# Kernel optimization log

Hardware: AMD Instinct MI355X
Metric: run time of the kernel (lower is better)

Reference implementation:

```python
import jax, jax.numpy as jnp
import numpy as np

P = 5            # assets (fixed by 5x5 MLP)
K = 4            # stacked layers
LB, UB = 0.0, 0.5
RF = 1.03
B = 524288       # batch size
ALPHA, OMEGA, BETA, MU = 0.1, 0.05, 0.05, 0.01
MAX_REBAL_ITERS = 8  # water-filling clamp loop converges in a few iters for P=5


def setup_inputs() -> dict:
    key = jax.random.key(0)
    k1, k2, k3, k4 = jax.random.split(key, 4)
    x1 = jax.random.uniform(k1, (B,), dtype=jnp.float32)                 # wealth per sample
    x2 = jax.random.uniform(k2, (B, P, P), dtype=jnp.float32)            # prev covariance
    eps = jax.random.normal(k3, (K, B, P), dtype=jnp.float32)            # N(0,I) draw per layer
    W = jax.random.normal(k4, (K, 3, P, P), dtype=jnp.float32) * 0.5     # 3 bias-free Linear(5,5) per layer
    return {"x1": x1, "x2": x2, "eps": eps, "W": W}


def _rebalance(w):
    """Vectorized clamp/redistribute loop over the whole batch. w: (B,P)."""
    old = w
    new = jnp.clip(w, LB, UB)
    done = jnp.zeros(w.shape[0], dtype=bool)

    def body(carry, _):
        old, new, done = carry
        leftover = jnp.sum(old - new, axis=1, keepdims=True)            # (B,1)
        masked = jnp.where(new != UB, new, 0.0)                          # non-capped weights
        new2 = new + leftover * masked / jnp.sum(masked, axis=1, keepdims=True)
        cont = jnp.any(new2 > UB, axis=1)                                # (B,)
        new3 = jnp.where(cont[:, None], jnp.clip(new2, LB, UB), new2)
        # freeze rows that already converged
        old_n = jnp.where(done[:, None], old, new2)
        new_n = jnp.where(done[:, None], new, new3)
        return (old_n, new_n, done | ~cont), None

    (_, new, _), _ = jax.lax.scan(body, (old, new, done), None, length=MAX_REBAL_ITERS)
    return new


def reference(x1, x2, eps, W):
    # Replicates the original bug: every StackLayer consumes the ORIGINAL
    # (x1, x2); only the last layer's output is returned.
    for k in range(K):
        Ce = jnp.einsum('bij,bj->bi', x2, eps[k])                        # prev_cov @ eps, (B,P)
        curr_cov = OMEGA + ALPHA * x2 + BETA * (Ce ** 2)[:, None, :]     # (B,P,P), row-broadcast
        R = MU + Ce                                                      # (B,P)
        h = R
        for l in range(3):                                               # torch Linear: x @ W.T
            h = jnp.tanh(h @ W[k, l].T)
        wts = jax.nn.softmax(h, axis=1)
        wts = _rebalance(wts)
        wealth = jnp.sum(x1[:, None] * wts * (1.0 + R) * RF, axis=1)     # (B,)
    return wealth, curr_cov
```

## Files before the change

### kernel.cpp

```cpp
#include <hip/hip_runtime.h>
#include <cmath>

#define P 5
#define LBV 0.0f
#define UBV 0.5f
#define RFV 1.03f
#define ALPHA 0.1f
#define OMEGA 0.05f
#define BETA 0.05f
#define MU 0.01f
#define NTHR 256

__device__ __forceinline__ float fast_tanh(float x) {
    float ax = fabsf(x);
    float t  = __expf(-2.0f * ax);
    float r  = (1.0f - t) * __builtin_amdgcn_rcpf(1.0f + t);
    return copysignf(r, x);
}

__global__ __launch_bounds__(NTHR) void portfolio_kernel(
    const float* __restrict__ x1,
    const float* __restrict__ x2,
    const float* __restrict__ eps,
    const float* __restrict__ W,
    float* __restrict__ out, int B)
{
    __shared__ float sW[3 * P * P];
    __shared__ float sX2[NTHR * P * P];
    __shared__ float sE[NTHR * P];

    const int tid = threadIdx.x;
    const int b0  = blockIdx.x * NTHR;

    if (tid < 3 * P * P) sW[tid] = W[3 * 3 * P * P + tid];

    const float* gx2 = x2 + (size_t)b0 * (P * P);
    #pragma unroll
    for (int i = 0; i < P * P; ++i)
        sX2[i * NTHR + tid] = gx2[i * NTHR + tid];

    const float* ge = eps + (size_t)3 * B * P + (size_t)b0 * P;
    #pragma unroll
    for (int i = 0; i < P; ++i)
        sE[i * NTHR + tid] = ge[i * NTHR + tid];

    __syncthreads();

    float* row = &sX2[tid * (P * P)];
    float r2[P * P];
    #pragma unroll
    for (int i = 0; i < P * P; ++i) r2[i] = row[i];

    float e[P];
    #pragma unroll
    for (int j = 0; j < P; ++j) e[j] = sE[tid * P + j];

    float Ce[P];
    #pragma unroll
    for (int i = 0; i < P; ++i) {
        float s = 0.0f;
        #pragma unroll
        for (int j = 0; j < P; ++j) s = fmaf(r2[i * P + j], e[j], s);
        Ce[i] = s;
    }

    float R[P], h[P];
    #pragma unroll
    for (int i = 0; i < P; ++i) { R[i] = MU + Ce[i]; h[i] = R[i]; }

    #pragma unroll
    for (int l = 0; l < 3; ++l) {
        float hn[P];
        #pragma unroll
        for (int i = 0; i < P; ++i) {
            float s = 0.0f;
            #pragma unroll
            for (int j = 0; j < P; ++j) s = fmaf(h[j], sW[l * P * P + i * P + j], s);
            hn[i] = fast_tanh(s);
        }
        #pragma unroll
        for (int i = 0; i < P; ++i) h[i] = hn[i];
    }

    float w[P], ssum = 0.0f;
    #pragma unroll
    for (int i = 0; i < P; ++i) { w[i] = __expf(h[i]); ssum += w[i]; }
    float rs = __builtin_amdgcn_rcpf(ssum);
    #pragma unroll
    for (int i = 0; i < P; ++i) w[i] *= rs;

    float oldv[P], nw[P];
    #pragma unroll
    for (int i = 0; i < P; ++i) {
        oldv[i] = w[i];
        nw[i]   = fminf(fmaxf(w[i], LBV), UBV);
    }
    #pragma unroll
    for (int it = 0; it < 8; ++it) {
        float leftover = 0.0f;
        #pragma unroll
        for (int i = 0; i < P; ++i) leftover += oldv[i] - nw[i];
        float mk[P], msum = 0.0f;
        #pragma unroll
        for (int i = 0; i < P; ++i) {
            mk[i] = (nw[i] != UBV) ? nw[i] : 0.0f;
            msum += mk[i];
        }
        float scale = leftover * __builtin_amdgcn_rcpf(msum);
        float n2[P];
        #pragma unroll
        for (int i = 0; i < P; ++i) n2[i] = fmaf(scale, mk[i], nw[i]);
        bool cont = false;
        #pragma unroll
        for (int i = 0; i < P; ++i) cont = cont || (n2[i] > UBV);
        #pragma unroll
        for (int i = 0; i < P; ++i) {
            oldv[i] = n2[i];
            nw[i]   = cont ? fminf(fmaxf(n2[i], LBV), UBV) : n2[i];
        }
        if (!cont) break;
    }

    float x1v = x1[b0 + tid];
    float ws = 0.0f;
    #pragma unroll
    for (int i = 0; i < P; ++i) ws = fmaf(nw[i], 1.0f + R[i], ws);
    out[b0 + tid] = x1v * ws * RFV;

    float ce2[P];
    #pragma unroll
    for (int j = 0; j < P; ++j) ce2[j] = Ce[j] * Ce[j];
    #pragma unroll
    for (int i = 0; i < P; ++i) {
        #pragma unroll
        for (int j = 0; j < P; ++j)
            row[i * P + j] = fmaf(BETA, ce2[j], fmaf(ALPHA, r2[i * P + j], OMEGA));
    }

    __syncthreads();

    float* gout = out + B + (size_t)b0 * (P * P);
    #pragma unroll
    for (int i = 0; i < P * P; ++i)
        gout[i * NTHR + tid] = sX2[i * NTHR + tid];
}

extern "C" void kernel_launch(void* const* d_in, const int* in_sizes, int n_in,
                              void* d_out, int out_size, void* d_ws, size_t ws_size,
                              hipStream_t stream) {
    const float* x1  = (const float*)d_in[0];
    const float* x2  = (const float*)d_in[1];
    const float* eps = (const float*)d_in[2];
    const float* W   = (const float*)d_in[3];
    float* out = (float*)d_out;
    const int B = in_sizes[0];
    const int blocks = B / NTHR;
    portfolio_kernel<<<blocks, NTHR, 0, stream>>>(x1, x2, eps, W, out, B);
}
```

Before: 134.5 us.

## Stage covariance via direct global-to-LDS loads and write output straight to global

Replaces the per-thread global-to-shared copy of the 256x25 covariance tile with global_load_lds 16-byte async copies straight into LDS. Eps and x1 are now loaded directly into registers per thread, and the weight matrices are read from global memory instead of shared memory. The output covariance is written directly from registers with a strided per-thread store, which drops the second barrier and LDS round trip but gives uncoalesced 100-byte-strided stores. It also adds a min-blocks-per-CU launch bound of 5 to raise occupancy.

```diff
diff --git a/kernel.cpp b/kernel.cpp
--- a/kernel.cpp
+++ b/kernel.cpp
@@ -11,6 +11,9 @@
 #define MU 0.01f
 #define NTHR 256
 
+#define AS1 __attribute__((address_space(1)))
+#define AS3 __attribute__((address_space(3)))
+
 __device__ __forceinline__ float fast_tanh(float x) {
     float ax = fabsf(x);
     float t  = __expf(-2.0f * ax);
@@ -18,42 +21,42 @@
     return copysignf(r, x);
 }
 
-__global__ __launch_bounds__(NTHR) void portfolio_kernel(
+__global__ __launch_bounds__(NTHR, 5) void portfolio_kernel(
     const float* __restrict__ x1,
     const float* __restrict__ x2,
     const float* __restrict__ eps,
     const float* __restrict__ W,
     float* __restrict__ out, int B)
 {
-    __shared__ float sW[3 * P * P];
     __shared__ float sX2[NTHR * P * P];
-    __shared__ float sE[NTHR * P];
 
-    const int tid = threadIdx.x;
-    const int b0  = blockIdx.x * NTHR;
+    const int tid  = threadIdx.x;
+    const int b0   = blockIdx.x * NTHR;
+    const int lane = tid & 63;
+    const int wv   = tid >> 6;
 
-    if (tid < 3 * P * P) sW[tid] = W[3 * 3 * P * P + tid];
+    float x1v = x1[b0 + tid];
+    const float* ge = eps + (size_t)3 * B * P + (size_t)(b0 + tid) * P;
+    float e[P];
+    #pragma unroll
+    for (int j = 0; j < P; ++j) e[j] = ge[j];
 
     const float* gx2 = x2 + (size_t)b0 * (P * P);
     #pragma unroll
-    for (int i = 0; i < P * P; ++i)
-        sX2[i * NTHR + tid] = gx2[i * NTHR + tid];
-
-    const float* ge = eps + (size_t)3 * B * P + (size_t)b0 * P;
-    #pragma unroll
-    for (int i = 0; i < P; ++i)
-        sE[i * NTHR + tid] = ge[i * NTHR + tid];
-
+    for (int i = 0; i < 6; ++i) {
+        int c = (i * 4 + wv) * 256;
+        __builtin_amdgcn_global_load_lds((const AS1 void*)(gx2 + c + lane * 4),
+                                         (AS3 void*)(&sX2[c]), 16, 0, 0);
+    }
+    if (wv == 0) {
+        __builtin_amdgcn_global_load_lds((const AS1 void*)(gx2 + 6144 + lane * 4),
+                                         (AS3 void*)(&sX2[6144]), 16, 0, 0);
+    }
     __syncthreads();
 
-    float* row = &sX2[tid * (P * P)];
     float r2[P * P];
     #pragma unroll
-    for (int i = 0; i < P * P; ++i) r2[i] = row[i];
-
-    float e[P];
-    #pragma unroll
-    for (int j = 0; j < P; ++j) e[j] = sE[tid * P + j];
+    for (int i = 0; i < P * P; ++i) r2[i] = sX2[tid * (P * P) + i];
 
     float Ce[P];
     #pragma unroll
@@ -68,6 +71,7 @@
     #pragma unroll
     for (int i = 0; i < P; ++i) { R[i] = MU + Ce[i]; h[i] = R[i]; }
 
+    const float* Wl = W + 3 * 3 * P * P;
     #pragma unroll
     for (int l = 0; l < 3; ++l) {
         float hn[P];
@@ -75,7 +79,7 @@
         for (int i = 0; i < P; ++i) {
             float s = 0.0f;
             #pragma unroll
-            for (int j = 0; j < P; ++j) s = fmaf(h[j], sW[l * P * P + i * P + j], s);
+            for (int j = 0; j < P; ++j) s = fmaf(h[j], Wl[l * P * P + i * P + j], s);
             hn[i] = fast_tanh(s);
         }
         #pragma unroll
@@ -121,7 +125,6 @@
         if (!cont) break;
     }
 
-    float x1v = x1[b0 + tid];
     float ws = 0.0f;
     #pragma unroll
     for (int i = 0; i < P; ++i) ws = fmaf(nw[i], 1.0f + R[i], ws);
@@ -130,19 +133,13 @@
     float ce2[P];
     #pragma unroll
     for (int j = 0; j < P; ++j) ce2[j] = Ce[j] * Ce[j];
+    float* gout = out + B + (size_t)(b0 + tid) * (P * P);
     #pragma unroll
     for (int i = 0; i < P; ++i) {
         #pragma unroll
         for (int j = 0; j < P; ++j)
-            row[i * P + j] = fmaf(BETA, ce2[j], fmaf(ALPHA, r2[i * P + j], OMEGA));
+            gout[i * P + j] = fmaf(BETA, ce2[j], fmaf(ALPHA, r2[i * P + j], OMEGA));
     }
-
-    __syncthreads();
-
-    float* gout = out + B + (size_t)b0 * (P * P);
-    #pragma unroll
-    for (int i = 0; i < P * P; ++i)
-        gout[i * NTHR + tid] = sX2[i * NTHR + tid];
 }
 
 extern "C" void kernel_launch(void* const* d_in, const int* in_sizes, int n_in,
```

Measured after the change: 142.5 us. +6.0%, slower.
